# Optimization experiments

Hardware: AMD Instinct MI355X
Metric: run time of the kernel (lower is better)

Reference implementation:

```python
import jax, jax.numpy as jnp
import numpy as np

B, L, D, E, H, FFN_MULT = 16, 2048, 512, 8, 8, 4
HD = D // H
ALPHA, BETA, LN_EPS = 1.0, 0.5, 1e-5


def _ln(x, g, b):
    mu = x.mean(-1, keepdims=True)
    var = ((x - mu) ** 2).mean(-1, keepdims=True)
    return (x - mu) * jax.lax.rsqrt(var + LN_EPS) * g + b


def setup_inputs() -> dict:
    key = jax.random.key(0)
    ks = jax.random.split(key, 20)
    s = 0.02
    return {
        "query": jax.random.normal(ks[0], (B, D), jnp.float32),
        "retrieved": jax.random.normal(ks[1], (B, L, D), jnp.float32),
        "w_gate": jax.random.normal(ks[2], (D, E), jnp.float32) * s,
        "ln_q_g": jnp.ones((E, D), jnp.float32),
        "ln_q_b": jnp.zeros((E, D), jnp.float32),
        "Wq": jax.random.normal(ks[3], (E, D, D), jnp.float32) * s,
        "bq": jnp.zeros((E, D), jnp.float32),
        "Wk": jax.random.normal(ks[4], (E, D, D), jnp.float32) * s,
        "bk": jnp.zeros((E, D), jnp.float32),
        "Wv": jax.random.normal(ks[5], (E, D, D), jnp.float32) * s,
        "bv": jnp.zeros((E, D), jnp.float32),
        "Wo": jax.random.normal(ks[6], (E, D, D), jnp.float32) * s,
        "bo": jnp.zeros((E, D), jnp.float32),
        "ln_o_g": jnp.ones((E, D), jnp.float32),
        "ln_o_b": jnp.zeros((E, D), jnp.float32),
        "W1": jax.random.normal(ks[7], (E, D, FFN_MULT * D), jnp.float32) * s,
        "b1": jnp.zeros((E, FFN_MULT * D), jnp.float32),
        "W2": jax.random.normal(ks[8], (E, FFN_MULT * D, D), jnp.float32) * s,
        "b2": jnpp_zeros((E, D)) if False else jnp.zeros((E, D), jnp.float32),
    }


def reference(query, retrieved, w_gate, ln_q_g, ln_q_b, Wq, bq, Wk, bk, Wv, bv,
              Wo, bo, ln_o_g, ln_o_b, W1, b1, W2, b2):
    # Gating (eval mode: no noise, r=None) -> (B, E)
    gates = jax.nn.softmax(query @ w_gate, axis=-1)

    # Per-expert LayerNorm of the (shared) query: normalize once, affine per expert
    mu = query.mean(-1, keepdims=True)
    var = ((query - mu) ** 2).mean(-1, keepdims=True)
    xn = (query - mu) * jax.lax.rsqrt(var + LN_EPS)              # (B, D)
    qn = xn[:, None, :] * ln_q_g[None] + ln_q_b[None]            # (B, E, D)

    # Cross-attention, query length 1, per expert (MHA with in/out proj)
    qh = (jnp.einsum('bed,edk->bek', qn, Wq) + bq).reshape(B, E, H, HD)
    k = (jnp.einsum('bld,edk->belk', retrieved, Wk) + bk[:, None, :]).reshape(B, E, L, H, HD)
    v = (jnp.einsum('bld,edk->belk', retrieved, Wv) + bv[:, None, :]).reshape(B, E, L, H, HD)
    scores = jnp.einsum('behc,belhc->behl', qh, k) / jnp.sqrt(jnp.float32(HD))
    probs = jax.nn.softmax(scores, axis=-1)                      # (B, E, H, L)
    attn = jnp.einsum('behl,belhc->behc', probs, v).reshape(B, E, D)
    attn_out = jnp.einsum('bed,edk->bek', attn, Wo) + bo         # (B, E, D)
    avg_probs = probs.mean(axis=2)                               # (B, E, L) heads averaged

    # Residual + FFN (dropouts inactive at eval)
    x = query[:, None, :] + attn_out                             # (B, E, D)
    xo = _ln(x, ln_o_g[None], ln_o_b[None])
    h = jax.nn.gelu(jnp.einsum('bed,edf->bef', xo, W1) + b1, approximate=False)
    y = jnp.einsum('bef,efd->bed', h, W2) + b2 + x               # expert_outs (B, E, D)

    # Entropy-derived reliability
    p = jnp.clip(avg_probs, 1e-12, None)
    Hent = -(p * jnp.log(p)).sum(-1)                             # (B, E)
    s_all = jnp.exp(-BETA * Hent)

    gt = gates * s_all
    gt = gt / (gt.sum(-1, keepdims=True) + 1e-9)
    mixture = (gt[..., None] * y).sum(1)                         # (B, D)
    fused = ALPHA * mixture + (1.0 - ALPHA) * query
    return fused, y, gt
```

## Files before the change

kernel.cpp:

```cpp
#include <hip/hip_runtime.h>
#include <math.h>

#define CB 16
#define CL 2048
#define CD 512
#define CE 8
#define CH 8
#define CEH 64
#define CF 2048

typedef __bf16 bf16x8 __attribute__((ext_vector_type(8)));
typedef float f32x4 __attribute__((ext_vector_type(4)));

#define GLL16(srcp, dstp) __builtin_amdgcn_global_load_lds( \
    (const __attribute__((address_space(1))) unsigned int*)(srcp), \
    (__attribute__((address_space(3))) unsigned int*)(dstp), 16, 0, 0)

#define WS_GATES 0
#define WS_XN    (WS_GATES + CB*CE)
#define WS_QN    (WS_XN + CB*CD)
#define WS_QH    (WS_QN + CB*CE*CD)
#define WS_SBIAS (WS_QH + CB*CE*CD)
#define WS_WK    (WS_SBIAS + CB*CE*CH)
#define WS_SC    (WS_WK + CB*CEH*CD)
#define WS_PART  WS_SC
#define WS_PART1 (WS_PART + 524288)
#define WS_ENT   (WS_SC + CB*CL*CEH)
#define WS_ATTN  (WS_ENT + CB*CE*8)
#define WS_X     (WS_ATTN + CB*CE*CD)
#define WS_XO    (WS_X + CB*CE*CD)
#define WS_HB    (WS_XO + CB*CE*CD)
#define WS_RP    (WS_HB + CB*CE*CF)
#define WS_PB16  (WS_RP + 8*CB*CEH*CD)

__global__ __launch_bounds__(256) void gstream_wq(
    const float* __restrict__ q, const float* __restrict__ g,
    const float* __restrict__ bln, const float* __restrict__ W,
    float* __restrict__ P) {
  int e = blockIdx.y;
  int nt = blockIdx.x % 8, kc = blockIdx.x / 8;
  int n0 = nt * 64, k0 = kc * 64;
  __shared__ float xs[64][20];
  __shared__ float red[16][64];
  __shared__ float muS[16], rsS[16];
  int t = threadIdx.x;
  {
    int b = t >> 4, j = t & 15;
    float s1 = 0.f, s2 = 0.f;
    const float* qb = q + b*CD + j*32;
    #pragma unroll
    for (int i = 0; i < 32; i++) { float v = qb[i]; s1 += v; s2 += v*v; }
    #pragma unroll
    for (int m = 1; m <= 8; m <<= 1) { s1 += __shfl_xor(s1, m); s2 += __shfl_xor(s2, m); }
    if (j == 0) {
      float mu = s1 * (1.0f/CD);
      float var = s2 * (1.0f/CD) - mu*mu;
      muS[b] = mu;
      rsS[b] = rsqrtf(var + 1e-5f);
    }
  }
  __syncthreads();
  for (int idx = t; idx < 64*16; idx += 256) {
    int k = idx & 63, b = idx >> 6;
    xs[k][b] = (q[b*CD + k0 + k] - muS[b]) * rsS[b] * g[e*CD + k0 + k] + bln[e*CD + k0 + k];
  }
  __syncthreads();
  int n = t & 63, kq = t >> 6;
  float acc[16] = {};
  const float* Wp = W + (size_t)e*CD*CD + (size_t)k0*CD + n0 + n;
  #pragma unroll 4
  for (int k = kq*16; k < kq*16 + 16; k++) {
    float w = Wp[(size_t)k * CD];
    const float4* xp = reinterpret_cast<const float4*>(&xs[k][0]);
    float4 x0 = xp[0], x1 = xp[1], x2 = xp[2], x3 = xp[3];
    acc[0]  += x0.x*w; acc[1]  += x0.y*w; acc[2]  += x0.z*w; acc[3]  += x0.w*w;
    acc[4]  += x1.x*w; acc[5]  += x1.y*w; acc[6]  += x1.z*w; acc[7]  += x1.w*w;
    acc[8]  += x2.x*w; acc[9]  += x2.y*w; acc[10] += x2.z*w; acc[11] += x2.w*w;
    acc[12] += x3.x*w; acc[13] += x3.y*w; acc[14] += x3.z*w; acc[15] += x3.w*w;
  }
  if (kq == 0) {
    #pragma unroll
    for (int b = 0; b < 16; b++) red[b][n] = acc[b];
  }
  __syncthreads();
  #pragma unroll
  for (int qq = 1; qq < 4; qq++) {
    if (kq == qq) {
      #pragma unroll
      for (int b = 0; b < 16; b++) red[b][n] += acc[b];
    }
    __syncthreads();
  }
  #pragma unroll
  for (int i = 0; i < 4; i++) {
    int b = kq*4 + i;
    P[(size_t)kc*65536 + (size_t)b*4096 + (size_t)e*512 + n0 + n] = red[b][n];
  }
}

template<int KC>
__global__ __launch_bounds__(256) void gstream(
    const float* __restrict__ X, int xb_, int xe_,
    const float* __restrict__ W, size_t we_, int ldw,
    float* __restrict__ P, int ntiles, size_t pc_, int pb_, int pe_) {
  int e = blockIdx.y;
  int nt = blockIdx.x % ntiles, kc = blockIdx.x / ntiles;
  int n0 = nt * 64, k0 = kc * KC;
  __shared__ float xs[KC][16];
  __shared__ float red[16][64];
  int t = threadIdx.x;
  for (int idx = t; idx < KC * 16; idx += 256) {
    int k = idx >> 4, b = idx & 15;
    xs[k][b] = X[(size_t)b * xb_ + (size_t)e * xe_ + k0 + k];
  }
  __syncthreads();
  int n = t & 63, kq = t >> 6;
  float acc[16] = {};
  const float* Wp = W + (size_t)e * we_ + (size_t)k0 * ldw + n0 + n;
  #pragma unroll 4
  for (int k = kq * (KC/4); k < (kq+1) * (KC/4); k++) {
    float w = Wp[(size_t)k * ldw];
    const float4* xp = reinterpret_cast<const float4*>(xs[k]);
    float4 x0 = xp[0], x1 = xp[1], x2 = xp[2], x3 = xp[3];
    acc[0]  += x0.x*w; acc[1]  += x0.y*w; acc[2]  += x0.z*w; acc[3]  += x0.w*w;
    acc[4]  += x1.x*w; acc[5]  += x1.y*w; acc[6]  += x1.z*w; acc[7]  += x1.w*w;
    acc[8]  += x2.x*w; acc[9]  += x2.y*w; acc[10] += x2.z*w; acc[11] += x2.w*w;
    acc[12] += x3.x*w; acc[13] += x3.y*w; acc[14] += x3.z*w; acc[15] += x3.w*w;
  }
  if (kq == 0) {
    #pragma unroll
    for (int b = 0; b < 16; b++) red[b][n] = acc[b];
  }
  __syncthreads();
  #pragma unroll
  for (int qq = 1; qq < 4; qq++) {
    if (kq == qq) {
      #pragma unroll
      for (int b = 0; b < 16; b++) red[b][n] += acc[b];
    }
    __syncthreads();
  }
  #pragma unroll
  for (int i = 0; i < 4; i++) {
    int b = kq*4 + i;
    P[(size_t)kc*pc_ + (size_t)b*pb_ + (size_t)e*pe_ + n0 + n] = red[b][n];
  }
}

__global__ __launch_bounds__(256) void gstream_v(
    const float* __restrict__ rp, const float* __restrict__ Wv,
    float* __restrict__ P) {
  int eh = blockIdx.y, kc = blockIdx.x;
  int e = eh >> 3, h = eh & 7;
  int k0 = kc * 64;
  __shared__ float xs[64][20];
  __shared__ float red[16][64];
  int t = threadIdx.x;
  for (int idx = t; idx < 64 * 16; idx += 256) {
    int k = idx & 63, b = idx >> 6;
    float s = 0.f;
    #pragma unroll
    for (int c = 0; c < 4; c++)
      s += rp[(size_t)c*(CB*CEH*CD) + ((size_t)(b*CEH + eh))*CD + k0 + k];
    xs[k][b] = s;
  }
  __syncthreads();
  int n = t & 63, kq = t >> 6;
  float acc[16] = {};
  const float* Wp = Wv + (size_t)e*CD*CD + (size_t)k0*CD + h*64 + n;
  #pragma unroll 4
  for (int k = kq*16; k < kq*16 + 16; k++) {
    float w = Wp[(size_t)k * CD];
    const float4* xp = reinterpret_cast<const float4*>(&xs[k][0]);
    float4 x0 = xp[0], x1 = xp[1], x2 = xp[2], x3 = xp[3];
    acc[0]  += x0.x*w; acc[1]  += x0.y*w; acc[2]  += x0.z*w; acc[3]  += x0.w*w;
    acc[4]  += x1.x*w; acc[5]  += x1.y*w; acc[6]  += x1.z*w; acc[7]  += x1.w*w;
    acc[8]  += x2.x*w; acc[9]  += x2.y*w; acc[10] += x2.z*w; acc[11] += x2.w*w;
    acc[12] += x3.x*w; acc[13] += x3.y*w; acc[14] += x3.z*w; acc[15] += x3.w*w;
  }
  if (kq == 0) { 
    #pragma unroll
    for (int b = 0; b < 16; b++) red[b][n] = acc[b]; }
  __syncthreads();
  #pragma unroll
  for (int qq = 1; qq < 4; qq++) {
    if (kq == qq) {
      #pragma unroll
      for (int b = 0; b < 16; b++) red[b][n] += acc[b];
    }
    __syncthreads();
  }
  #pragma unroll
  for (int i = 0; i < 4; i++) {
    int b = kq*4 + i;
    P[(size_t)kc*65536 + (size_t)b*4096 + (size_t)eh*64 + n] = red[b][n];
  }
}

__global__ __launch_bounds__(256) void gstream_wo(
    const float* __restrict__ Pv, const float* __restrict__ bv,
    const float* __restrict__ Wo, float* __restrict__ P) {
  int e = blockIdx.y;
  int nt = blockIdx.x % 8, kc = blockIdx.x / 8;
  int n0 = nt * 64, k0 = kc * 64;
  __shared__ float xs[64][20];
  __shared__ float red[16][64];
  int t = threadIdx.x;
  for (int idx = t; idx < 64 * 16; idx += 256) {
    int k = idx & 63, b = idx >> 6;
    float s = bv[e*CD + k0 + k];
    #pragma unroll
    for (int c = 0; c < 8; c++)
      s += Pv[(size_t)c*65536 + (size_t)b*4096 + e*512 + k0 + k];
    xs[k][b] = s;
  }
  __syncthreads();
  int n = t & 63, kq = t >> 6;
  float acc[16] = {};
  const float* Wp = Wo + (size_t)e*CD*CD + (size_t)k0*CD + n0 + n;
  #pragma unroll 4
  for (int k = kq*16; k < kq*16 + 16; k++) {
    float w = Wp[(size_t)k * CD];
    const float4* xp = reinterpret_cast<const float4*>(&xs[k][0]);
    float4 x0 = xp[0], x1 = xp[1], x2 = xp[2], x3 = xp[3];
    acc[0]  += x0.x*w; acc[1]  += x0.y*w; acc[2]  += x0.z*w; acc[3]  += x0.w*w;
    acc[4]  += x1.x*w; acc[5]  += x1.y*w; acc[6]  += x1.z*w; acc[7]  += x1.w*w;
    acc[8]  += x2.x*w; acc[9]  += x2.y*w; acc[10] += x2.z*w; acc[11] += x2.w*w;
    acc[12] += x3.x*w; acc[13] += x3.y*w; acc[14] += x3.z*w; acc[15] += x3.w*w;
  }
  if (kq == 0) {
    #pragma unroll
    for (int b = 0; b < 16; b++) red[b][n] = acc[b]; }
  __syncthreads();
  #pragma unroll
  for (int qq = 1; qq < 4; qq++) {
    if (kq == qq) {
      #pragma unroll
      for (int b = 0; b < 16; b++) red[b][n] += acc[b];
    }
    __syncthreads();
  }
  #pragma unroll
  for (int i = 0; i < 4; i++) {
    int b = kq*4 + i;
    P[(size_t)kc*65536 + (size_t)b*4096 + (size_t)e*512 + n0 + n] = red[b][n];
  }
}

__global__ __launch_bounds__(256) void gstream_w2(
    const float* __restrict__ P1, const float* __restrict__ b1,
    const float* __restrict__ W2, float* __restrict__ Pout) {
  int e = blockIdx.y;
  int nt = blockIdx.x % 8, kc = blockIdx.x / 8;
  int n0 = nt * 64, k0 = kc * 256;
  __shared__ float xs[256][20];
  __shared__ float red[16][64];
  int t = threadIdx.x;
  for (int idx = t; idx < 256 * 16; idx += 256) {
    int k = idx & 255, b = idx >> 8;
    float v = b1[e*CF + k0 + k];
    #pragma unroll
    for (int c = 0; c < 4; c++)
      v += P1[(size_t)c*262144 + (size_t)b*16384 + e*2048 + k0 + k];
    xs[k][b] = 0.5f*v*(1.f + erff(v*0.70710678118f));
  }
  __syncthreads();
  int n = t & 63, kq = t >> 6;
  float acc[16] = {};
  const float* Wp = W2 + (size_t)e*CF*CD + (size_t)k0*CD + n0 + n;
  #pragma unroll 4
  for (int k = kq*64; k < kq*64 + 64; k++) {
    float w = Wp[(size_t)k * CD];
    const float4* xp = reinterpret_cast<const float4*>(&xs[k][0]);
    float4 x0 = xp[0], x1 = xp[1], x2 = xp[2], x3 = xp[3];
    acc[0]  += x0.x*w; acc[1]  += x0.y*w; acc[2]  += x0.z*w; acc[3]  += x0.w*w;
    acc[4]  += x1.x*w; acc[5]  += x1.y*w; acc[6]  += x1.z*w; acc[7]  += x1.w*w;
    acc[8]  += x2.x*w; acc[9]  += x2.y*w; acc[10] += x2.z*w; acc[11] += x2.w*w;
    acc[12] += x3.x*w; acc[13] += x3.y*w; acc[14] += x3.z*w; acc[15] += x3.w*w;
  }
  if (kq == 0) {
    #pragma unroll
    for (int b = 0; b < 16; b++) red[b][n] = acc[b]; }
  __syncthreads();
  #pragma unroll
  for (int qq = 1; qq < 4; qq++) {
    if (kq == qq) {
      #pragma unroll
      for (int b = 0; b < 16; b++) red[b][n] += acc[b];
    }
    __syncthreads();
  }
  #pragma unroll
  for (int i = 0; i < 4; i++) {
    int b = kq*4 + i;
    Pout[(size_t)kc*65536 + (size_t)b*4096 + (size_t)e*512 + n0 + n] = red[b][n];
  }
}

__global__ __launch_bounds__(512) void comb_o_lno(
    const float* __restrict__ P, const float* __restrict__ bo,
    const float* __restrict__ q, const float* __restrict__ g,
    const float* __restrict__ bb, float* __restrict__ xb,
    float* __restrict__ xo) {
  int be = blockIdx.x, b = be >> 3, e = be & 7, t = threadIdx.x;
  float v = q[b*CD + t] + bo[e*CD + t];
  #pragma unroll
  for (int c = 0; c < 8; c++)
    v += P[(size_t)c*65536 + (size_t)b*4096 + e*512 + t];
  xb[be*CD + t] = v;
  __shared__ float red[512];
  red[t] = v; __syncthreads();
  for (int s = 256; s > 0; s >>= 1) { if (t < s) red[t] += red[t+s]; __syncthreads(); }
  float mu = red[0] * (1.0f/CD); __syncthreads();
  float c0 = v - mu;
  red[t] = c0*c0; __syncthreads();
  for (int s = 256; s > 0; s >>= 1) { if (t < s) red[t] += red[t+s]; __syncthreads(); }
  float rstd = rsqrtf(red[0] * (1.0f/CD) + 1e-5f);
  xo[be*CD + t] = c0*rstd*g[e*CD + t] + bb[e*CD + t];
}

__global__ __launch_bounds__(512) void comb_ffn2_final(
    const float* __restrict__ P, const float* __restrict__ b2,
    const float* __restrict__ xb, const float* __restrict__ q,
    const float* __restrict__ wg, const float* __restrict__ entp,
    float* __restrict__ yout, float* __restrict__ fused,
    float* __restrict__ gtout) {
  int b = blockIdx.x, t = threadIdx.x;
  int w = t >> 6, lane = t & 63;
  __shared__ float gpart[8][8];
  __shared__ float gt_s[CE];
  float ge[CE];
  {
    float qv = q[b*CD + t];
    #pragma unroll
    for (int e = 0; e < CE; e++) ge[e] = qv * wg[t*CE + e];
  }
  #pragma unroll
  for (int m = 32; m >= 1; m >>= 1) {
    #pragma unroll
    for (int e = 0; e < CE; e++) ge[e] += __shfl_xor(ge[e], m);
  }
  if (lane == 0) {
    #pragma unroll
    for (int e = 0; e < CE; e++) gpart[w][e] = ge[e];
  }
  __syncthreads();
  if (t == 0) {
    float logit[CE];
    float m = -1e30f;
    #pragma unroll
    for (int e = 0; e < CE; e++) {
      float s = 0.f;
      #pragma unroll
      for (int ww = 0; ww < 8; ww++) s += gpart[ww][e];
      logit[e] = s;
      m = fmaxf(m, s);
    }
    float ssum = 0.f, ex[CE];
    #pragma unroll
    for (int e = 0; e < CE; e++) { ex[e] = __expf(logit[e] - m); ssum += ex[e]; }
    float s2 = 0.f;
    #pragma unroll
    for (int e = 0; e < CE; e++) {
      float Hs = 0.f;
      #pragma unroll
      for (int c = 0; c < 8; c++) Hs += entp[(b*CE + e)*8 + c];
      gt_s[e] = (ex[e]/ssum) * __expf(-0.5f * Hs);
      s2 += gt_s[e];
    }
    s2 += 1e-9f;
    #pragma unroll
    for (int e = 0; e < CE; e++) gt_s[e] /= s2;
  }
  __syncthreads();
  float acc = 0.f;
  #pragma unroll
  for (int e = 0; e < CE; e++) {
    float y = b2[e*CD + t] + xb[(b*CE + e)*CD + t];
    #pragma unroll
    for (int c = 0; c < 8; c++)
      y += P[(size_t)c*65536 + (size_t)b*4096 + e*512 + t];
    yout[(b*CE + e)*CD + t] = y;
    acc += gt_s[e] * y;
  }
  fused[b*CD + t] = acc;
  if (t < CE) gtout[b*CE + t] = gt_s[t];
}

__global__ __launch_bounds__(256) void k4_wkeff(
    const float* __restrict__ Wk, const float* __restrict__ Pq,
    const float* __restrict__ bq, const float* __restrict__ bk,
    __bf16* __restrict__ wkh, float* __restrict__ sbias) {
  int e = blockIdx.y;
  int h = blockIdx.x >> 3, dt = blockIdx.x & 7;
  int d0 = dt * 64;
  __shared__ float wks[64][65];
  __shared__ float qs[64][20];
  __shared__ float red[16][64];
  int t = threadIdx.x;
  for (int idx = t; idx < 64*64; idx += 256) {
    int c = idx & 63, d = idx >> 6;
    wks[c][d] = Wk[(size_t)e*CD*CD + (size_t)(d0+d)*CD + h*64 + c];
  }
  for (int idx = t; idx < 64*16; idx += 256) {
    int c = idx & 63, b = idx >> 6;
    float s = bq[e*CD + h*64 + c];
    #pragma unroll
    for (int cc = 0; cc < 8; cc++)
      s += Pq[(size_t)cc*65536 + (size_t)b*4096 + e*512 + h*64 + c];
    qs[c][b] = s;
  }
  __syncthreads();
  if (dt == 0) {
    int bb = t >> 4, ii = t & 15;
    float p = 0.f;
    #pragma unroll
    for (int j = 0; j < 4; j++)
      p += qs[ii*4 + j][bb] * bk[e*CD + h*64 + ii*4 + j];
    p += __shfl_xor(p, 1);
    p += __shfl_xor(p, 2);
    p += __shfl_xor(p, 4);
    p += __shfl_xor(p, 8);
    if (ii == 0) sbias[bb*CEH + e*8 + h] = p;
  }
  int d = t & 63, cq = t >> 6;
  float acc[16] = {};
  #pragma unroll 4
  for (int c = cq*16; c < cq*16 + 16; c++) {
    float w = wks[c][d];
    const float4* xp = reinterpret_cast<const float4*>(&qs[c][0]);
    float4 x0 = xp[0], x1 = xp[1], x2 = xp[2], x3 = xp[3];
    acc[0]  += x0.x*w; acc[1]  += x0.y*w; acc[2]  += x0.z*w; acc[3]  += x0.w*w;
    acc[4]  += x1.x*w; acc[5]  += x1.y*w; acc[6]  += x1.z*w; acc[7]  += x1.w*w;
    acc[8]  += x2.x*w; acc[9]  += x2.y*w; acc[10] += x2.z*w; acc[11] += x2.w*w;
    acc[12] += x3.x*w; acc[13] += x3.y*w; acc[14] += x3.z*w; acc[15] += x3.w*w;
  }
  if (cq == 0) { 
    #pragma unroll
    for (int b = 0; b < 16; b++) red[b][d] = acc[b]; }
  __syncthreads();
  #pragma unroll
  for (int qq = 1; qq < 4; qq++) {
    if (cq == qq) {
      #pragma unroll
      for (int b = 0; b < 16; b++) red[b][d] += acc[b];
    }
    __syncthreads();
  }
  int eh = e*8 + h;
  #pragma unroll
  for (int i = 0; i < 4; i++) {
    int b = cq*4 + i;
    wkh[((size_t)(b*CEH + eh))*CD + d0 + d] = (__bf16)red[b][d];
  }
}

__global__ __launch_bounds__(256) void k5_mfma(
    const float* __restrict__ ret, const __bf16* __restrict__ wkh,
    const float* __restrict__ sbias, float* __restrict__ sc,
    float* __restrict__ lmax, float* __restrict__ lsum) {
  int b = blockIdx.y, lt = blockIdx.x, t = threadIdx.x;
  int w = t >> 6, lane = t & 63;
  int lnlo = lane & 15, lnhi = lane >> 4;
  int lh = w & 1, ehh = w >> 1;
  int l0blk = lt*32;
  int ehbase = ehh*32;
  __shared__ __align__(16) char ldsbuf[32768];
  f32x4 acc[2];
  acc[0] = (f32x4){0.f,0.f,0.f,0.f};
  acc[1] = (f32x4){0.f,0.f,0.f,0.f};
  const float*  retb  = ret + (size_t)(b*CL + l0blk)*CD;
  const __bf16* wkhb  = wkh + (size_t)b*CEH*CD;

  int rs0 = t,        rl0 = rs0 >> 4, rg0 = ((rs0 & 15) ^ (rl0 & 15)) << 2;
  int rs1 = t + 256,  rl1 = rs1 >> 4, rg1 = ((rs1 & 15) ^ (rl1 & 15)) << 2;
  int ws0 = t,        we0 = ws0 >> 3, wg0 = ((ws0 & 7) ^ (we0 & 7)) << 3;
  int ws1 = t + 256,  we1 = ws1 >> 3, wg1 = ((ws1 & 7) ^ (we1 & 7)) << 3;

  #define K5_STAGE(bufi, kt) do {                                          \
    char* rB = ldsbuf + (bufi)*8192;                                       \
    char* wB = ldsbuf + 16384 + (bufi)*8192;                               \
    int dofs = (kt)*64;                                                    \
    GLL16(retb + (size_t)rl0*CD + dofs + rg0, rB + rs0*16);                \
    GLL16(retb + (size_t)rl1*CD + dofs + rg1, rB + rs1*16);                \
    GLL16(wkhb + (size_t)we0*CD + dofs + wg0, wB + ws0*16);                \
    GLL16(wkhb + (size_t)we1*CD + dofs + wg1, wB + ws1*16);                \
  } while (0)

  K5_STAGE(0, 0);
  __syncthreads();
  #pragma unroll
  for (int kt = 0; kt < 8; kt++) {
    int cur = kt & 1;
    if (kt < 7) K5_STAGE(cur ^ 1, kt + 1);
    const char* rB = ldsbuf + cur*8192;
    const char* wB = ldsbuf + 16384 + cur*8192;
    #pragma unroll
    for (int sub = 0; sub < 2; sub++) {
      int g0 = (sub*8 + lnhi*2 + 0) ^ lnlo;
      int g1 = (sub*8 + lnhi*2 + 1) ^ lnlo;
      float4 f0 = *reinterpret_cast<const float4*>(rB + (lh*16 + lnlo)*256 + g0*16);
      float4 f1 = *reinterpret_cast<const float4*>(rB + (lh*16 + lnlo)*256 + g1*16);
      bf16x8 bfrag;
      bfrag[0]=(__bf16)f0.x; bfrag[1]=(__bf16)f0.y; bfrag[2]=(__bf16)f0.z; bfrag[3]=(__bf16)f0.w;
      bfrag[4]=(__bf16)f1.x; bfrag[5]=(__bf16)f1.y; bfrag[6]=(__bf16)f1.z; bfrag[7]=(__bf16)f1.w;
      int ga = (sub*4 + lnhi) ^ (lnlo & 7);
      bf16x8 a0 = *reinterpret_cast<const bf16x8*>(wB + (ehbase + 0*16 + lnlo)*128 + ga*16);
      bf16x8 a1 = *reinterpret_cast<const bf16x8*>(wB + (ehbase + 1*16 + lnlo)*128 + ga*16);
      acc[0] = __builtin_amdgcn_mfma_f32_16x16x32_bf16(a0, bfrag, acc[0], 0, 0, 0);
      acc[1] = __builtin_amdgcn_mfma_f32_16x16x32_bf16(a1, bfrag, acc[1], 0, 0, 0);
    }
    __syncthreads();
  }
  #undef K5_STAGE

  int strip = lt*2 + lh;
  int l = l0blk + lh*16 + lnlo;
  #pragma unroll
  for (int et = 0; et < 2; et++) {
    #pragma unroll
    for (int i = 0; i < 4; i++) {
      int eh = ehbase + et*16 + lnhi*4 + i;
      float v = acc[et][i]*0.125f + sbias[b*CEH + eh]*0.125f;
      sc[((size_t)(b*CEH + eh))*CL + l] = v;
      float m = v;
      m = fmaxf(m, __shfl_xor(m, 1));
      m = fmaxf(m, __shfl_xor(m, 2));
      m = fmaxf(m, __shfl_xor(m, 4));
      m = fmaxf(m, __shfl_xor(m, 8));
      float s = __expf(v - m);
      s += __shfl_xor(s, 1);
      s += __shfl_xor(s, 2);
      s += __shfl_xor(s, 4);
      s += __shfl_xor(s, 8);
      if (lnlo == et*4 + i) {
        lmax[((size_t)(b*CEH + eh))*128 + strip] = m;
        lsum[((size_t)(b*CEH + eh))*128 + strip] = s;
      }
    }
  }
}

__global__ __launch_bounds__(256) void k5n(
    const float* __restrict__ sc, const float* __restrict__ lmax,
    const float* __restrict__ lsum, __bf16* __restrict__ pb,
    float* __restrict__ entp) {
  int e = blockIdx.x, b = blockIdx.y, lc = blockIdx.z, t = threadIdx.x;
  __shared__ float M_s[8], I_s[8];
  {
    int g = t >> 5, lane = t & 31;
    int eh = e*8 + g;
    const float* lm = lmax + ((size_t)(b*CEH + eh))*128;
    const float* ls = lsum + ((size_t)(b*CEH + eh))*128;
    float M = -1e30f, S = 0.f;
    #pragma unroll
    for (int j = 0; j < 4; j++) {
      float m2 = lm[lane + j*32], s2 = ls[lane + j*32];
      float Mn = fmaxf(M, m2);
      S = S*__expf(M - Mn) + s2*__expf(m2 - Mn);
      M = Mn;
    }
    #pragma unroll
    for (int mask = 16; mask >= 1; mask >>= 1) {
      float Mo = __shfl_xor(M, mask), So = __shfl_xor(S, mask);
      float Mn = fmaxf(M, Mo);
      S = S*__expf(M - Mn) + So*__expf(Mo - Mn);
      M = Mn;
    }
    if (lane == 0) { M_s[g] = M; I_s[g] = 1.f / S; }
  }
  __syncthreads();
  int l = lc*256 + t;
  float pbav = 0.f;
  #pragma unroll
  for (int h = 0; h < 8; h++) {
    size_t ix = ((size_t)(b*CEH + e*8 + h))*CL + l;
    float p = __expf(sc[ix] - M_s[h]) * I_s[h];
    pb[ix] = (__bf16)p;
    pbav += p;
  }
  pbav = fmaxf(pbav*0.125f, 1e-12f);
  float ent = -pbav * __logf(pbav);
  __shared__ float red[256];
  red[t] = ent; __syncthreads();
  for (int s = 128; s > 0; s >>= 1) { if (t < s) red[t] += red[t+s]; __syncthreads(); }
  if (t == 0) entp[(b*CE + e)*8 + lc] = red[0];
}

__global__ __launch_bounds__(256) void k6_mfma(
    const __bf16* __restrict__ pb, const float* __restrict__ ret,
    float* __restrict__ part) {
  int b = blockIdx.y;
  int dt = blockIdx.x & 7, lc = blockIdx.x >> 3;
  int d0 = dt*64, l0 = lc*512;
  int t = threadIdx.x, w = t >> 6, lane = t & 63;
  int lnlo = lane & 15, lnhi = lane >> 4;
  __shared__ __bf16 Bs[2][64][40];
  f32x4 acc[4];
  #pragma unroll
  for (int et = 0; et < 4; et++) acc[et] = (f32x4){0.f,0.f,0.f,0.f};
  const __bf16* pbb = pb + ((size_t)(b*CEH) + lnlo)*CL + l0 + lnhi*8;
  int srow = t & 31, scol = (t >> 5)*8;
  const float* retb = ret + ((size_t)(b*CL) + l0 + srow)*CD + d0 + scol;
  float4 v0 = *reinterpret_cast<const float4*>(retb);
  float4 v1 = *reinterpret_cast<const float4*>(retb + 4);
  bf16x8 ap0 = *reinterpret_cast<const bf16x8*>(pbb);
  bf16x8 ap1 = *reinterpret_cast<const bf16x8*>(pbb + (size_t)16*CL);
  bf16x8 ap2 = *reinterpret_cast<const bf16x8*>(pbb + (size_t)32*CL);
  bf16x8 ap3 = *reinterpret_cast<const bf16x8*>(pbb + (size_t)48*CL);
  #pragma unroll
  for (int kt = 0; kt < 16; kt++) {
    int cur = kt & 1;
    Bs[cur][scol+0][srow] = (__bf16)v0.x; Bs[cur][scol+1][srow] = (__bf16)v0.y;
    Bs[cur][scol+2][srow] = (__bf16)v0.z; Bs[cur][scol+3][srow] = (__bf16)v0.w;
    Bs[cur][scol+4][srow] = (__bf16)v1.x; Bs[cur][scol+5][srow] = (__bf16)v1.y;
    Bs[cur][scol+6][srow] = (__bf16)v1.z; Bs[cur][scol+7][srow] = (__bf16)v1.w;
    bf16x8 an0, an1, an2, an3;
    if (kt < 15) {
      v0 = *reinterpret_cast<const float4*>(retb + (size_t)(kt+1)*32*CD);
      v1 = *reinterpret_cast<const float4*>(retb + (size_t)(kt+1)*32*CD + 4);
      an0 = *reinterpret_cast<const bf16x8*>(pbb + (kt+1)*32);
      an1 = *reinterpret_cast<const bf16x8*>(pbb + (size_t)16*CL + (kt+1)*32);
      an2 = *reinterpret_cast<const bf16x8*>(pbb + (size_t)32*CL + (kt+1)*32);
      an3 = *reinterpret_cast<const bf16x8*>(pbb + (size_t)48*CL + (kt+1)*32);
    }
    __syncthreads();
    bf16x8 bfrag = *reinterpret_cast<const bf16x8*>(&Bs[cur][w*16 + lnlo][lnhi*8]);
    acc[0] = __builtin_amdgcn_mfma_f32_16x16x32_bf16(ap0, bfrag, acc[0], 0, 0, 0);
    acc[1] = __builtin_amdgcn_mfma_f32_16x16x32_bf16(ap1, bfrag, acc[1], 0, 0, 0);
    acc[2] = __builtin_amdgcn_mfma_f32_16x16x32_bf16(ap2, bfrag, acc[2], 0, 0, 0);
    acc[3] = __builtin_amdgcn_mfma_f32_16x16x32_bf16(ap3, bfrag, acc[3], 0, 0, 0);
    if (kt < 15) { ap0 = an0; ap1 = an1; ap2 = an2; ap3 = an3; }
    __syncthreads();
  }
  float* dst = part + (size_t)lc*(CB*CEH*CD);
  int d = d0 + w*16 + lnlo;
  #pragma unroll
  for (int et = 0; et < 4; et++) {
    #pragma unroll
    for (int i = 0; i < 4; i++) {
      int eh = et*16 + lnhi*4 + i;
      dst[((size_t)(b*CEH + eh))*CD + d] = acc[et][i];
    }
  }
}

extern "C" void kernel_launch(void* const* d_in, const int* in_sizes, int n_in,
                              void* d_out, int out_size, void* d_ws, size_t ws_size,
                              hipStream_t stream) {
  const float* q    = (const float*)d_in[0];
  const float* ret  = (const float*)d_in[1];
  const float* wg   = (const float*)d_in[2];
  const float* lnqg = (const float*)d_in[3];
  const float* lnqb = (const float*)d_in[4];
  const float* Wq   = (const float*)d_in[5];
  const float* bq   = (const float*)d_in[6];
  const float* Wk   = (const float*)d_in[7];
  const float* bk   = (const float*)d_in[8];
  const float* Wv   = (const float*)d_in[9];
  const float* bv   = (const float*)d_in[10];
  const float* Wo   = (const float*)d_in[11];
  const float* bo   = (const float*)d_in[12];
  const float* lnog = (const float*)d_in[13];
  const float* lnob = (const float*)d_in[14];
  const float* W1   = (const float*)d_in[15];
  const float* b1   = (const float*)d_in[16];
  const float* W2   = (const float*)d_in[17];
  const float* b2   = (const float*)d_in[18];

  float* ws = (float*)d_ws;
  float* fused = (float*)d_out;
  float* yout  = fused + CB*CD;
  float* gtout = yout + CB*CE*CD;

  float* sbias = ws + WS_SBIAS;
  __bf16* wkh  = (__bf16*)(ws + WS_WK);
  float* sc    = ws + WS_SC;
  float* part0 = ws + WS_PART;
  float* part1 = ws + WS_PART1;
  float* entp  = ws + WS_ENT;
  float* xb    = ws + WS_X;
  float* xo    = ws + WS_XO;
  float* rpart = ws + WS_RP;
  __bf16* pb16 = (__bf16*)(ws + WS_PB16);
  float* lmax  = rpart;
  float* lsum  = rpart + CB*CEH*128;

  gstream_wq<<<dim3(64, CE), 256, 0, stream>>>(q, lnqg, lnqb, Wq, part0);
  k4_wkeff<<<dim3(64, CE), 256, 0, stream>>>(Wk, part0, bq, bk, wkh, sbias);
  k5_mfma<<<dim3(64, CB), 256, 0, stream>>>(ret, wkh, sbias, sc, lmax, lsum);
  k5n<<<dim3(CE, CB, 8), 256, 0, stream>>>(sc, lmax, lsum, pb16, entp);
  k6_mfma<<<dim3(32, CB), 256, 0, stream>>>(pb16, ret, rpart);
  gstream_v<<<dim3(8, CEH), 256, 0, stream>>>(rpart, Wv, part1);
  gstream_wo<<<dim3(64, CE), 256, 0, stream>>>(part1, bv, Wo, part0);
  comb_o_lno<<<CB*CE, 512, 0, stream>>>(part0, bo, q, lnog, lnob, xb, xo);
  gstream<128><<<dim3(128, CE), 256, 0, stream>>>(xo, CE*CD, CD, W1, (size_t)CD*CF, CF,
                                                  part0, 32, 262144, CE*CF, CF);
  gstream_w2<<<dim3(64, CE), 256, 0, stream>>>(part0, b1, W2, rpart);
  comb_ffn2_final<<<CB, 512, 0, stream>>>(rpart, b2, xb, q, wg, entp, yout, fused, gtout);
}
```

Measured before the change: 119.0 us.

## Fuse output LayerNorm into W1 stream and store attention scores as bf16

The LayerNorm that followed the Wo combine is moved into the W1 GEMV kernel. Each block recomputes the per-row mean and variance from xb with a single-pass sum and sum-of-squares, then normalises while staging into shared memory. This drops the separate xo buffer and the LDS tree reductions in the combine kernel. Separately, the attention scores sc are written as bf16 instead of fp32, halving score traffic between k5 and k5n, at the cost of score precision in the softmax and of redundant LayerNorm statistics computed in every W1 block.

```diff
diff --git a/kernel.cpp b/kernel.cpp
--- a/kernel.cpp
+++ b/kernel.cpp
@@ -98,29 +98,46 @@
   }
 }
 
-template<int KC>
-__global__ __launch_bounds__(256) void gstream(
-    const float* __restrict__ X, int xb_, int xe_,
-    const float* __restrict__ W, size_t we_, int ldw,
-    float* __restrict__ P, int ntiles, size_t pc_, int pb_, int pe_) {
+__global__ __launch_bounds__(256) void gstream_w1(
+    const float* __restrict__ xb, const float* __restrict__ g,
+    const float* __restrict__ bb, const float* __restrict__ W1,
+    float* __restrict__ P) {
   int e = blockIdx.y;
-  int nt = blockIdx.x % ntiles, kc = blockIdx.x / ntiles;
-  int n0 = nt * 64, k0 = kc * KC;
-  __shared__ float xs[KC][16];
+  int nt = blockIdx.x % 32, kc = blockIdx.x / 32;
+  int n0 = nt * 64, k0 = kc * 128;
+  __shared__ float xs[128][20];
   __shared__ float red[16][64];
+  __shared__ float muS[16], rsS[16];
   int t = threadIdx.x;
-  for (int idx = t; idx < KC * 16; idx += 256) {
-    int k = idx >> 4, b = idx & 15;
-    xs[k][b] = X[(size_t)b * xb_ + (size_t)e * xe_ + k0 + k];
+  {
+    int b = t >> 4, j = t & 15;
+    float s1 = 0.f, s2 = 0.f;
+    const float* xr = xb + (size_t)(b*CE + e)*CD + j*32;
+    #pragma unroll
+    for (int i = 0; i < 32; i++) { float v = xr[i]; s1 += v; s2 += v*v; }
+    #pragma unroll
+    for (int m = 1; m <= 8; m <<= 1) { s1 += __shfl_xor(s1, m); s2 += __shfl_xor(s2, m); }
+    if (j == 0) {
+      float mu = s1 * (1.0f/CD);
+      float var = s2 * (1.0f/CD) - mu*mu;
+      muS[b] = mu;
+      rsS[b] = rsqrtf(var + 1e-5f);
+    }
+  }
+  __syncthreads();
+  for (int idx = t; idx < 128*16; idx += 256) {
+    int k = idx & 127, b = idx >> 7;
+    xs[k][b] = (xb[(size_t)(b*CE + e)*CD + k0 + k] - muS[b]) * rsS[b] * g[e*CD + k0 + k]
+               + bb[e*CD + k0 + k];
   }
   __syncthreads();
   int n = t & 63, kq = t >> 6;
   float acc[16] = {};
-  const float* Wp = W + (size_t)e * we_ + (size_t)k0 * ldw + n0 + n;
+  const float* Wp = W1 + (size_t)e*CD*CF + (size_t)k0*CF + n0 + n;
   #pragma unroll 4
-  for (int k = kq * (KC/4); k < (kq+1) * (KC/4); k++) {
-    float w = Wp[(size_t)k * ldw];
-    const float4* xp = reinterpret_cast<const float4*>(xs[k]);
+  for (int k = kq*32; k < kq*32 + 32; k++) {
+    float w = Wp[(size_t)k * CF];
+    const float4* xp = reinterpret_cast<const float4*>(&xs[k][0]);
     float4 x0 = xp[0], x1 = xp[1], x2 = xp[2], x3 = xp[3];
     acc[0]  += x0.x*w; acc[1]  += x0.y*w; acc[2]  += x0.z*w; acc[3]  += x0.w*w;
     acc[4]  += x1.x*w; acc[5]  += x1.y*w; acc[6]  += x1.z*w; acc[7]  += x1.w*w;
@@ -143,7 +160,7 @@
   #pragma unroll
   for (int i = 0; i < 4; i++) {
     int b = kq*4 + i;
-    P[(size_t)kc*pc_ + (size_t)b*pb_ + (size_t)e*pe_ + n0 + n] = red[b][n];
+    P[(size_t)kc*262144 + (size_t)b*16384 + (size_t)e*2048 + n0 + n] = red[b][n];
   }
 }
 
@@ -297,26 +314,15 @@
   }
 }
 
-__global__ __launch_bounds__(512) void comb_o_lno(
+__global__ __launch_bounds__(512) void comb_o(
     const float* __restrict__ P, const float* __restrict__ bo,
-    const float* __restrict__ q, const float* __restrict__ g,
-    const float* __restrict__ bb, float* __restrict__ xb,
-    float* __restrict__ xo) {
+    const float* __restrict__ q, float* __restrict__ xb) {
   int be = blockIdx.x, b = be >> 3, e = be & 7, t = threadIdx.x;
   float v = q[b*CD + t] + bo[e*CD + t];
   #pragma unroll
   for (int c = 0; c < 8; c++)
     v += P[(size_t)c*65536 + (size_t)b*4096 + e*512 + t];
   xb[be*CD + t] = v;
-  __shared__ float red[512];
-  red[t] = v; __syncthreads();
-  for (int s = 256; s > 0; s >>= 1) { if (t < s) red[t] += red[t+s]; __syncthreads(); }
-  float mu = red[0] * (1.0f/CD); __syncthreads();
-  float c0 = v - mu;
-  red[t] = c0*c0; __syncthreads();
-  for (int s = 256; s > 0; s >>= 1) { if (t < s) red[t] += red[t+s]; __syncthreads(); }
-  float rstd = rsqrtf(red[0] * (1.0f/CD) + 1e-5f);
-  xo[be*CD + t] = c0*rstd*g[e*CD + t] + bb[e*CD + t];
 }
 
 __global__ __launch_bounds__(512) void comb_ffn2_final(
@@ -457,7 +463,7 @@
 
 __global__ __launch_bounds__(256) void k5_mfma(
     const float* __restrict__ ret, const __bf16* __restrict__ wkh,
-    const float* __restrict__ sbias, float* __restrict__ sc,
+    const float* __restrict__ sbias, __bf16* __restrict__ sc,
     float* __restrict__ lmax, float* __restrict__ lsum) {
   int b = blockIdx.y, lt = blockIdx.x, t = threadIdx.x;
   int w = t >> 6, lane = t & 63;
@@ -522,13 +528,15 @@
     for (int i = 0; i < 4; i++) {
       int eh = ehbase + et*16 + lnhi*4 + i;
       float v = acc[et][i]*0.125f + sbias[b*CEH + eh]*0.125f;
-      sc[((size_t)(b*CEH + eh))*CL + l] = v;
-      float m = v;
+      __bf16 vb = (__bf16)v;
+      sc[((size_t)(b*CEH + eh))*CL + l] = vb;
+      float vq = (float)vb;
+      float m = vq;
       m = fmaxf(m, __shfl_xor(m, 1));
       m = fmaxf(m, __shfl_xor(m, 2));
       m = fmaxf(m, __shfl_xor(m, 4));
       m = fmaxf(m, __shfl_xor(m, 8));
-      float s = __expf(v - m);
+      float s = __expf(vq - m);
       s += __shfl_xor(s, 1);
       s += __shfl_xor(s, 2);
       s += __shfl_xor(s, 4);
@@ -542,7 +550,7 @@
 }
 
 __global__ __launch_bounds__(256) void k5n(
-    const float* __restrict__ sc, const float* __restrict__ lmax,
+    const __bf16* __restrict__ sc, const float* __restrict__ lmax,
     const float* __restrict__ lsum, __bf16* __restrict__ pb,
     float* __restrict__ entp) {
   int e = blockIdx.x, b = blockIdx.y, lc = blockIdx.z, t = threadIdx.x;
@@ -575,7 +583,7 @@
   #pragma unroll
   for (int h = 0; h < 8; h++) {
     size_t ix = ((size_t)(b*CEH + e*8 + h))*CL + l;
-    float p = __expf(sc[ix] - M_s[h]) * I_s[h];
+    float p = __expf((float)sc[ix] - M_s[h]) * I_s[h];
     pb[ix] = (__bf16)p;
     pbav += p;
   }
@@ -675,12 +683,11 @@
 
   float* sbias = ws + WS_SBIAS;
   __bf16* wkh  = (__bf16*)(ws + WS_WK);
-  float* sc    = ws + WS_SC;
+  __bf16* sc   = (__bf16*)(ws + WS_SC);
   float* part0 = ws + WS_PART;
   float* part1 = ws + WS_PART1;
   float* entp  = ws + WS_ENT;
   float* xb    = ws + WS_X;
-  float* xo    = ws + WS_XO;
   float* rpart = ws + WS_RP;
   __bf16* pb16 = (__bf16*)(ws + WS_PB16);
   float* lmax  = rpart;
@@ -693,9 +700,8 @@
   k6_mfma<<<dim3(32, CB), 256, 0, stream>>>(pb16, ret, rpart);
   gstream_v<<<dim3(8, CEH), 256, 0, stream>>>(rpart, Wv, part1);
   gstream_wo<<<dim3(64, CE), 256, 0, stream>>>(part1, bv, Wo, part0);
-  comb_o_lno<<<CB*CE, 512, 0, stream>>>(part0, bo, q, lnog, lnob, xb, xo);
-  gstream<128><<<dim3(128, CE), 256, 0, stream>>>(xo, CE*CD, CD, W1, (size_t)CD*CF, CF,
-                                                  part0, 32, 262144, CE*CF, CF);
+  comb_o<<<CB*CE, 512, 0, stream>>>(part0, bo, q, xb);
+  gstream_w1<<<dim3(128, CE), 256, 0, stream>>>(xb, lnog, lnob, W1, part0);
   gstream_w2<<<dim3(64, CE), 256, 0, stream>>>(part0, b1, W2, rpart);
   comb_ffn2_final<<<CB, 512, 0, stream>>>(rpart, b2, xb, q, wg, entp, yout, fused, gtout);
 }
```

After: 118.8 us. No clear change (-0.2%).
